# Performance work log

Hardware: AMD Instinct MI355X
Metric: run time of the kernel (lower is better)

Reference implementation:

```python
import jax, jax.numpy as jnp
import numpy as np


def setup_inputs() -> dict:
    key = jax.random.key(0)
    k1, k2 = jax.random.split(key)
    d, T, n = 256, 8192, 64
    # scale down so exp(ht^T D^T D hj) stays in range, as typical trained D would
    H = jax.random.normal(k1, (d, T), dtype=jnp.float32) * 0.1
    D = jax.random.normal(k2, (n, d), dtype=jnp.float32) * 0.1
    l2 = jnp.ones((), dtype=jnp.float32)
    return {"H": H, "D": D, "l2": l2}


def reference(H, D, l2):
    # H: [d, T], D: [n, d]
    DH = D @ H                                   # [n, T] = D @ H_T.T
    # S[t, j] = h_t^T (D^T D) h_j  == (DH)^T (DH)
    S = jnp.einsum('nt,nj->tj', DH, DH)          # [T, T]
    # beta_j = exp(-0.5 * ||D h_j||^2); row t: attn[t,:] = beta * exp(S[t,:]) / sum
    log_beta = -0.5 * jnp.sum(DH * DH, axis=0)   # [T]
    attn_map = jax.nn.softmax(S + log_beta[None, :], axis=1)  # [T, T]
    Z = l2 * (H @ attn_map)                      # [d, T]
    return Z
```

## Files before the change

### kernel.cpp

```cpp
#include <hip/hip_runtime.h>

#define T_DIM 8192
#define D_DIM 256
#define N_DIM 64
#define LOG2E 1.44269504f

typedef __bf16 bf16x8 __attribute__((ext_vector_type(8)));
typedef __bf16 bf16x4 __attribute__((ext_vector_type(4)));
typedef float f32x16 __attribute__((ext_vector_type(16)));

__device__ __forceinline__ f32x16 zero16() {
  f32x16 v;
#pragma unroll
  for (int i = 0; i < 16; ++i) v[i] = 0.f;
  return v;
}


__global__ __launch_bounds__(256) void k_dh(const float* __restrict__ H,
                                            const float* __restrict__ Dm,
                                            __bf16* __restrict__ DHf,
                                            float* __restrict__ lbe,
                                            float* __restrict__ rowsum) {
  __shared__ __bf16 HlThi[64 * 264];
  __shared__ __bf16 HlTlo[64 * 264];
  __shared__ __bf16 DHs[64 * 72];
  const int tid = threadIdx.x;
  const int t0 = blockIdx.x * 64;
  const int lane = tid & 63;
  const int wave = tid >> 6;
  const int h = lane >> 5;
  const int l31 = lane & 31;
  const float4* H4 = (const float4*)H;
#pragma unroll
  for (int r = 0; r < 16; ++r) {
    int idx = r * 256 + tid;
    int d = idx >> 4, tc = idx & 15;
    float4 v = H4[(size_t)d * (T_DIM / 4) + (t0 >> 2) + tc];
    float vv[4] = {v.x, v.y, v.z, v.w};
#pragma unroll
    for (int i = 0; i < 4; ++i) {
      __bf16 hi = (__bf16)vv[i];
      float lo = vv[i] - (float)hi;
      HlThi[(tc * 4 + i) * 264 + d] = hi;
      HlTlo[(tc * 4 + i) * 264 + d] = (__bf16)lo;
    }
  }
  __syncthreads();
  const int tt = wave & 1, nh = wave >> 1;
  const int m = tt * 32 + l31;
  const int n = nh * 32 + l31;
  f32x16 c = zero16();
  for (int kk = 0; kk < 16; ++kk) {
    bf16x8 ahi = *(const bf16x8*)&HlThi[m * 264 + kk * 16 + h * 8];
    bf16x8 alo = *(const bf16x8*)&HlTlo[m * 264 + kk * 16 + h * 8];
    const float4* dp = (const float4*)(Dm + (size_t)n * 256 + kk * 16 + h * 8);
    float4 b0 = dp[0], b1 = dp[1];
    float bv[8] = {b0.x, b0.y, b0.z, b0.w, b1.x, b1.y, b1.z, b1.w};
    bf16x8 bhi, blo;
#pragma unroll
    for (int i = 0; i < 8; ++i) {
      __bf16 hi = (__bf16)bv[i];
      bhi[i] = hi;
      blo[i] = (__bf16)(bv[i] - (float)hi);
    }
    c = __builtin_amdgcn_mfma_f32_32x32x16_bf16(ahi, bhi, c, 0, 0, 0);
    c = __builtin_amdgcn_mfma_f32_32x32x16_bf16(ahi, blo, c, 0, 0, 0);
    c = __builtin_amdgcn_mfma_f32_32x32x16_bf16(alo, bhi, c, 0, 0, 0);
  }
#pragma unroll
  for (int r = 0; r < 16; ++r) {
    int row = tt * 32 + (r & 3) + 8 * (r >> 2) + 4 * h;
    DHs[row * 72 + n] = (__bf16)c[r];
  }
  __syncthreads();
#pragma unroll
  for (int r = 0; r < 2; ++r) {
    int idx = r * 256 + tid;
    int g = idx >> 8, cc = (idx >> 5) & 7, l = idx & 31;
    bf16x8 w = *(const bf16x8*)&DHs[(g * 32 + l) * 72 + cc * 8];
    *(bf16x8*)(DHf + (size_t)(blockIdx.x * 2 + g) * 2048 + cc * 256 + l * 8) = w;
  }
  if (tid < 64) {
    float s = 0.f;
#pragma unroll
    for (int q = 0; q < 8; ++q) {
      bf16x8 w = *(const bf16x8*)&DHs[tid * 72 + q * 8];
#pragma unroll
      for (int i = 0; i < 8; ++i) { float f = (float)w[i]; s += f * f; }
    }
    lbe[t0 + tid] = -0.5f * s * LOG2E;
    rowsum[t0 + tid] = 0.f;
  }
}

__global__ __launch_bounds__(256, 2) void k_rowsum(const __bf16* __restrict__ DHf,
                                                   const float* __restrict__ lbe,
                                                   float* __restrict__ rowsum) {
  __shared__ float red2[64 * 65];
  const int tid = threadIdx.x;
  const int lane = tid & 63;
  const int wave = tid >> 6;
  const int h = lane >> 5;
  const int tt = wave & 1, jt = wave >> 1;
  const int t0 = (int)(blockIdx.x >> 4) * 64;
  const int jbase = (int)(blockIdx.x & 15) * 512;
  const int Gt = (t0 >> 5) + tt;
  bf16x8 aR[4];
#pragma unroll
  for (int kk = 0; kk < 4; ++kk)
    aR[kk] = *(const bf16x8*)(DHf + (size_t)Gt * 2048 + kk * 512 + lane * 8);
  float racc[16];
#pragma unroll
  for (int r = 0; r < 16; ++r) racc[r] = 0.f;
  for (int jit = 0; jit < 8; ++jit) {
    const size_t Gj = (jbase >> 5) + jit * 2 + jt;
    bf16x8 b[4];
#pragma unroll
    for (int kk = 0; kk < 4; ++kk)
      b[kk] = *(const bf16x8*)(DHf + Gj * 2048 + kk * 512 + lane * 8);
    const float lbv = lbe[jbase + jit * 64 + jt * 32 + (lane & 31)];
    f32x16 s = zero16();
#pragma unroll
    for (int kk = 0; kk < 4; ++kk)
      s = __builtin_amdgcn_mfma_f32_32x32x16_bf16(aR[kk], b[kk], s, 0, 0, 0);
#pragma unroll
    for (int r = 0; r < 16; ++r)
      racc[r] += __builtin_amdgcn_exp2f(__builtin_fmaf(s[r], LOG2E, lbv));
  }
#pragma unroll
  for (int r = 0; r < 16; ++r) {
    int tl = tt * 32 + (r & 3) + 8 * (r >> 2) + 4 * h;
    red2[tl * 65 + jt * 32 + (lane & 31)] = racc[r];
  }
  __syncthreads();
  if (tid < 64) {
    float s = 0.f;
#pragma unroll 8
    for (int c = 0; c < 64; ++c) s += red2[tid * 65 + c];
    atomicAdd(&rowsum[t0 + tid], s);
  }
}

__global__ __launch_bounds__(256) void k_scaleH(const float* __restrict__ H,
                                                const float* __restrict__ rowsum,
                                                __bf16* __restrict__ Hf,
                                                float* __restrict__ Z) {
  __shared__ float rinvL[64];
  const int tid = threadIdx.x;
  const int bx = blockIdx.x;
  const int tblk = bx >> 1, dh = bx & 1;
  const int t0 = tblk * 64;
  if (tid < 64) rinvL[tid] = 1.0f / rowsum[t0 + tid];
  __syncthreads();
#pragma unroll
  for (int itr = 0; itr < 4; ++itr) {
    int idx = itr * 256 + tid;
    int dl = idx >> 3, c = idx & 7;
    int d = dh * 128 + dl;
    int tloc = c * 8;
    const float4* hp = (const float4*)(H + (size_t)d * T_DIM + t0 + tloc);
    float4 v0 = hp[0], v1 = hp[1];
    float4 r0 = *(const float4*)&rinvL[tloc];
    float4 r1 = *(const float4*)&rinvL[tloc + 4];
    bf16x8 w;
    w[0] = (__bf16)(v0.x * r0.x); w[1] = (__bf16)(v0.y * r0.y);
    w[2] = (__bf16)(v0.z * r0.z); w[3] = (__bf16)(v0.w * r0.w);
    w[4] = (__bf16)(v1.x * r1.x); w[5] = (__bf16)(v1.y * r1.y);
    w[6] = (__bf16)(v1.z * r1.z); w[7] = (__bf16)(v1.w * r1.w);
    *(bf16x8*)(Hf + (size_t)(tblk * 8 + (d >> 5)) * 2048 + c * 256 + (d & 31) * 8) = w;
  }
  float4* Z4 = (float4*)Z;
  const int base = bx * 256 + tid;
  const float4 z4 = {0.f, 0.f, 0.f, 0.f};
#pragma unroll
  for (int r = 0; r < 8; ++r) Z4[r * 65536 + base] = z4;
}

__global__ __launch_bounds__(256, 3) void k_z(const __bf16* __restrict__ Hf,
                                              const __bf16* __restrict__ DHf,
                                              const float* __restrict__ lbe,
                                              const float* __restrict__ l2p,
                                              float* __restrict__ Z) {
  __shared__ __bf16 Pt[2][128 * 64];
  const int tid = threadIdx.x;
  const int lane = tid & 63;
  const int wave = tid >> 6;
  const int h = lane >> 5;
  const int l31 = lane & 31;
  const int bx = blockIdx.x;
  const int ts = bx & 3;
  const int dh = (bx >> 2) & 1;
  const int j0 = (bx >> 3) * 128;
  const int tbase = ts * 2048;
  const float l2v = l2p[0];
  const int s_tt = wave & 1, s_jg = wave >> 1;
  bf16x8 bS[2][4];
  float lbv[2];
#pragma unroll
  for (int q = 0; q < 2; ++q) {
    const size_t Gj = (j0 >> 5) + s_jg * 2 + q;
#pragma unroll
    for (int kk = 0; kk < 4; ++kk)
      bS[q][kk] = *(const bf16x8*)(DHf + Gj * 2048 + kk * 512 + lane * 8);
    lbv[q] = lbe[j0 + (s_jg * 2 + q) * 32 + l31];
  }
  f32x16 acc[2][2];
#pragma unroll
  for (int u = 0; u < 2; ++u)
#pragma unroll
    for (int v = 0; v < 2; ++v) acc[u][v] = zero16();

  bf16x8 aR[4];
#pragma unroll
  for (int kk = 0; kk < 4; ++kk)
    aR[kk] = *(const bf16x8*)(DHf + (size_t)(ts * 64 + s_tt) * 2048 + kk * 512 + lane * 8);

#define S_PHASE(p_, it_)                                                        \
  {                                                                             \
    _Pragma("unroll") for (int q = 0; q < 2; ++q) {                             \
      f32x16 s = zero16();                                                      \
      _Pragma("unroll") for (int kk = 0; kk < 4; ++kk)                          \
          s = __builtin_amdgcn_mfma_f32_32x32x16_bf16(aR[kk], bS[q][kk], s, 0,  \
                                                      0, 0);                    \
      const int jl = (s_jg * 2 + q) * 32 + l31;                                 \
      const int sj = (jl ^ (jl >> 3)) & 7;                                      \
      _Pragma("unroll") for (int g = 0; g < 4; ++g) {                           \
        const int tl = s_tt * 32 + g * 8 + 4 * h;                               \
        bf16x4 pv;                                                              \
        pv[0] = (__bf16)__builtin_amdgcn_exp2f(                                 \
            __builtin_fmaf(s[g * 4 + 0], LOG2E, lbv[q]));                       \
        pv[1] = (__bf16)__builtin_amdgcn_exp2f(                                 \
            __builtin_fmaf(s[g * 4 + 1], LOG2E, lbv[q]));                       \
        pv[2] = (__bf16)__builtin_amdgcn_exp2f(                                 \
            __builtin_fmaf(s[g * 4 + 2], LOG2E, lbv[q]));                       \
        pv[3] = (__bf16)__builtin_amdgcn_exp2f(                                 \
            __builtin_fmaf(s[g * 4 + 3], LOG2E, lbv[q]));                       \
        const int cchunk = tl >> 3;                                             \
        *(bf16x4*)&Pt[p_][jl * 64 + ((cchunk ^ sj) << 3) + 4 * h] = pv;         \
      }                                                                         \
    }                                                                           \
  }

  S_PHASE(0, 0);
#pragma unroll
  for (int kk = 0; kk < 4; ++kk)
    aR[kk] = *(const bf16x8*)(DHf + (size_t)(ts * 64 + 2 + s_tt) * 2048 + kk * 512 + lane * 8);

  for (int it = 0; it < 32; ++it) {
    const int p = it & 1;
    __syncthreads();
    if (it < 31) S_PHASE(p ^ 1, it + 1);
    if (it < 30) {
      const size_t Gt = ts * 64 + (it + 2) * 2 + s_tt;
#pragma unroll
      for (int kk = 0; kk < 4; ++kk)
        aR[kk] = *(const bf16x8*)(DHf + Gt * 2048 + kk * 512 + lane * 8);
    }
    const size_t hbase = (size_t)((ts * 32 + it) * 8) * 2048;
#pragma unroll
    for (int kk = 0; kk < 4; ++kk) {
      bf16x8 af[2], bw[2];
#pragma unroll
      for (int u = 0; u < 2; ++u) {
        const int dgrp = dh * 4 + (wave & 1) * 2 + u;
        af[u] = *(const bf16x8*)(Hf + hbase + (size_t)dgrp * 2048 + kk * 512 + lane * 8);
      }
      const int c = kk * 2 + h;
#pragma unroll
      for (int v = 0; v < 2; ++v) {
        int j = (wave >> 1) * 64 + v * 32 + l31;
        bw[v] = *(const bf16x8*)&Pt[p][j * 64 + ((c ^ ((j ^ (j >> 3)) & 7)) << 3)];
      }
#pragma unroll
      for (int u = 0; u < 2; ++u)
#pragma unroll
        for (int v = 0; v < 2; ++v)
          acc[u][v] = __builtin_amdgcn_mfma_f32_32x32x16_bf16(af[u], bw[v], acc[u][v], 0, 0, 0);
    }
  }
#undef S_PHASE
#pragma unroll
  for (int u = 0; u < 2; ++u)
#pragma unroll
    for (int v = 0; v < 2; ++v)
#pragma unroll
      for (int r = 0; r < 16; ++r) {
        int d = dh * 128 + (wave & 1) * 64 + u * 32 + (r & 3) + 8 * (r >> 2) + 4 * h;
        int j = j0 + (wave >> 1) * 64 + v * 32 + l31;
        atomicAdd(&Z[(size_t)d * T_DIM + j], acc[u][v][r] * l2v);
      }
}

extern "C" void kernel_launch(void* const* d_in, const int* in_sizes, int n_in,
                              void* d_out, int out_size, void* d_ws,
                              size_t ws_size, hipStream_t stream) {
  (void)in_sizes; (void)n_in; (void)out_size; (void)ws_size;
  const float* H = (const float*)d_in[0];
  const float* Dm = (const float*)d_in[1];
  const float* l2 = (const float*)d_in[2];
  float* Z = (float*)d_out;
  char* ws = (char*)d_ws;
  __bf16* DHf = (__bf16*)ws;
  float* lbe = (float*)(ws + 1048576);
  float* rowsum = (float*)(ws + 1048576 + 32768);
  __bf16* Hf = (__bf16*)(ws + 1048576 + 65536);

  k_dh<<<128, 256, 0, stream>>>(H, Dm, DHf, lbe, rowsum);
  k_rowsum<<<2048, 256, 0, stream>>>(DHf, lbe, rowsum);
  k_scaleH<<<256, 256, 0, stream>>>(H, rowsum, Hf, Z);
  k_z<<<512, 256, 0, stream>>>(Hf, DHf, lbe, l2, Z);
}
```

Baseline: 176.1 us.

## Stage scaled H tiles into LDS via async global_load_lds with swizzled layout

k_scaleH now writes the row-normalised bf16 H in a row-major, XOR-swizzled per-tile layout. k_z uses global_load_lds to bring each 128x64 H tile into a double-buffered LDS array and reads MFMA A fragments from LDS instead of from global memory. The goal is to overlap H loads with the S/exp phase and to make the global reads coalesced. LDS use per block doubles, so launch bounds drop from 3 to 2 blocks per CU, which costs occupancy. The barrier also moves to the end of each iteration.

```diff
diff --git a/kernel.cpp b/kernel.cpp
--- a/kernel.cpp
+++ b/kernel.cpp
@@ -144,7 +144,7 @@
 
 __global__ __launch_bounds__(256) void k_scaleH(const float* __restrict__ H,
                                                 const float* __restrict__ rowsum,
-                                                __bf16* __restrict__ Hf,
+                                                __bf16* __restrict__ Hbf_sw,
                                                 float* __restrict__ Z) {
   __shared__ float rinvL[64];
   const int tid = threadIdx.x;
@@ -156,9 +156,10 @@
 #pragma unroll
   for (int itr = 0; itr < 4; ++itr) {
     int idx = itr * 256 + tid;
-    int dl = idx >> 3, c = idx & 7;
+    int dl = idx >> 3, tbp = idx & 7;
     int d = dh * 128 + dl;
-    int tloc = c * 8;
+    int swz = (d ^ (d >> 3)) & 7;
+    int tloc = (tbp ^ swz) << 3;
     const float4* hp = (const float4*)(H + (size_t)d * T_DIM + t0 + tloc);
     float4 v0 = hp[0], v1 = hp[1];
     float4 r0 = *(const float4*)&rinvL[tloc];
@@ -168,7 +169,7 @@
     w[2] = (__bf16)(v0.z * r0.z); w[3] = (__bf16)(v0.w * r0.w);
     w[4] = (__bf16)(v1.x * r1.x); w[5] = (__bf16)(v1.y * r1.y);
     w[6] = (__bf16)(v1.z * r1.z); w[7] = (__bf16)(v1.w * r1.w);
-    *(bf16x8*)(Hf + (size_t)(tblk * 8 + (d >> 5)) * 2048 + c * 256 + (d & 31) * 8) = w;
+    *(bf16x8*)(Hbf_sw + (size_t)tblk * 16384 + (size_t)d * 64 + tbp * 8) = w;
   }
   float4* Z4 = (float4*)Z;
   const int base = bx * 256 + tid;
@@ -177,11 +178,12 @@
   for (int r = 0; r < 8; ++r) Z4[r * 65536 + base] = z4;
 }
 
-__global__ __launch_bounds__(256, 3) void k_z(const __bf16* __restrict__ Hf,
+__global__ __launch_bounds__(256, 2) void k_z(const __bf16* __restrict__ Hbf_sw,
                                               const __bf16* __restrict__ DHf,
                                               const float* __restrict__ lbe,
                                               const float* __restrict__ l2p,
                                               float* __restrict__ Z) {
+  __shared__ __bf16 Hs[2][128 * 64];
   __shared__ __bf16 Pt[2][128 * 64];
   const int tid = threadIdx.x;
   const int lane = tid & 63;
@@ -192,7 +194,6 @@
   const int ts = bx & 3;
   const int dh = (bx >> 2) & 1;
   const int j0 = (bx >> 3) * 128;
-  const int tbase = ts * 2048;
   const float l2v = l2p[0];
   const int s_tt = wave & 1, s_jg = wave >> 1;
   bf16x8 bS[2][4];
@@ -211,12 +212,22 @@
 #pragma unroll
     for (int v = 0; v < 2; ++v) acc[u][v] = zero16();
 
-  bf16x8 aR[4];
-#pragma unroll
-  for (int kk = 0; kk < 4; ++kk)
-    aR[kk] = *(const bf16x8*)(DHf + (size_t)(ts * 64 + s_tt) * 2048 + kk * 512 + lane * 8);
-
-#define S_PHASE(p_, it_)                                                        \
+#define DMA_HS(buf_, it_)                                                       \
+  {                                                                             \
+    const __bf16* gsrc =                                                        \
+        Hbf_sw + (size_t)(ts * 32 + (it_)) * 16384 + (size_t)dh * 8192;         \
+    _Pragma("unroll") for (int r = 0; r < 4; ++r) {                             \
+      int chunk = wave * 4 + r;                                                 \
+      __builtin_amdgcn_global_load_lds(                                         \
+          (const __attribute__((address_space(1))) unsigned int*)(gsrc +        \
+              chunk * 512 + lane * 8),                                          \
+          (__attribute__((address_space(3))) unsigned int*)(&Hs[buf_][0] +      \
+              chunk * 512),                                                     \
+          16, 0, 0);                                                            \
+    }                                                                           \
+  }
+
+#define S_PHASE(p_)                                                             \
   {                                                                             \
     _Pragma("unroll") for (int q = 0; q < 2; ++q) {                             \
       f32x16 s = zero16();                                                      \
@@ -242,31 +253,38 @@
     }                                                                           \
   }
 
-  S_PHASE(0, 0);
+  bf16x8 aR[4];
+#pragma unroll
+  for (int kk = 0; kk < 4; ++kk)
+    aR[kk] = *(const bf16x8*)(DHf + (size_t)(ts * 64 + s_tt) * 2048 + kk * 512 + lane * 8);
+  DMA_HS(0, 0);
+  S_PHASE(0);
 #pragma unroll
   for (int kk = 0; kk < 4; ++kk)
     aR[kk] = *(const bf16x8*)(DHf + (size_t)(ts * 64 + 2 + s_tt) * 2048 + kk * 512 + lane * 8);
+  __syncthreads();
 
   for (int it = 0; it < 32; ++it) {
     const int p = it & 1;
-    __syncthreads();
-    if (it < 31) S_PHASE(p ^ 1, it + 1);
+    if (it < 31) {
+      DMA_HS(p ^ 1, it + 1);
+      S_PHASE(p ^ 1);
+    }
     if (it < 30) {
       const size_t Gt = ts * 64 + (it + 2) * 2 + s_tt;
 #pragma unroll
       for (int kk = 0; kk < 4; ++kk)
         aR[kk] = *(const bf16x8*)(DHf + Gt * 2048 + kk * 512 + lane * 8);
     }
-    const size_t hbase = (size_t)((ts * 32 + it) * 8) * 2048;
 #pragma unroll
     for (int kk = 0; kk < 4; ++kk) {
+      const int c = kk * 2 + h;
       bf16x8 af[2], bw[2];
 #pragma unroll
       for (int u = 0; u < 2; ++u) {
-        const int dgrp = dh * 4 + (wave & 1) * 2 + u;
-        af[u] = *(const bf16x8*)(Hf + hbase + (size_t)dgrp * 2048 + kk * 512 + lane * 8);
+        int dl = (wave & 1) * 64 + u * 32 + l31;
+        af[u] = *(const bf16x8*)&Hs[p][dl * 64 + ((c ^ ((dl ^ (dl >> 3)) & 7)) << 3)];
       }
-      const int c = kk * 2 + h;
 #pragma unroll
       for (int v = 0; v < 2; ++v) {
         int j = (wave >> 1) * 64 + v * 32 + l31;
@@ -278,8 +296,10 @@
         for (int v = 0; v < 2; ++v)
           acc[u][v] = __builtin_amdgcn_mfma_f32_32x32x16_bf16(af[u], bw[v], acc[u][v], 0, 0, 0);
     }
+    __syncthreads();
   }
 #undef S_PHASE
+#undef DMA_HS
 #pragma unroll
   for (int u = 0; u < 2; ++u)
 #pragma unroll
@@ -304,10 +324,10 @@
   __bf16* DHf = (__bf16*)ws;
   float* lbe = (float*)(ws + 1048576);
   float* rowsum = (float*)(ws + 1048576 + 32768);
-  __bf16* Hf = (__bf16*)(ws + 1048576 + 65536);
+  __bf16* Hbf_sw = (__bf16*)(ws + 1048576 + 65536);
 
   k_dh<<<128, 256, 0, stream>>>(H, Dm, DHf, lbe, rowsum);
   k_rowsum<<<2048, 256, 0, stream>>>(DHf, lbe, rowsum);
-  k_scaleH<<<256, 256, 0, stream>>>(H, rowsum, Hf, Z);
-  k_z<<<512, 256, 0, stream>>>(Hf, DHf, lbe, l2, Z);
-}
+  k_scaleH<<<256, 256, 0, stream>>>(H, rowsum, Hbf_sw, Z);
+  k_z<<<512, 256, 0, stream>>>(Hbf_sw, DHf, lbe, l2, Z);
+}
```

Result: faster. 160.3 us (-8.9%).
